# Kernel tuning notes

Hardware: AMD Instinct MI355X
Metric: run time of the kernel (lower is better)

The kernel has to match this reference:

```python
import jax, jax.numpy as jnp
import numpy as np

B, C, T, H, W = 8, 3, 16, 64, 64
CIN = C * T          # 48, conv in_channels
CQK = CIN // 8       # 6, query/key channels


def setup_inputs() -> dict:
    key = jax.random.key(0)
    ks = jax.random.split(key, 8)
    s = 0.05
    return {
        "x": jax.random.normal(ks[0], (B, C, T, H, W), dtype=jnp.float32),
        "Wq": jax.random.normal(ks[1], (CQK, CIN), dtype=jnp.float32) * s,
        "bq": jax.random.normal(ks[2], (CQK,), dtype=jnp.float32) * s,
        "Wk": jax.random.normal(ks[3], (CQK, CIN), dtype=jnp.float32) * s,
        "bk": jax.random.normal(ks[4], (CQK,), dtype=jnp.float32) * s,
        "Wv": jax.random.normal(ks[5], (CIN, CIN), dtype=jnp.float32) * s,
        "bv": jax.random.normal(ks[6], (CIN,), dtype=jnp.float32) * s,
        "gamma": jax.random.normal(ks[7], (1,), dtype=jnp.float32) * s,
    }


def reference(x, Wq, bq, Wk, bk, Wv, bv, gamma):
    b, c, t, h, w = x.shape
    n = h * w
    # merge channel and time dims: [B, C*T, H*W]
    x2 = x.reshape(b, c * t, n)
    # 1x1 convs are per-position channel matmuls
    q = jnp.einsum('oc,bcn->bon', Wq, x2) + bq[None, :, None]   # [B, CQK, N]
    k = jnp.einsum('oc,bcn->bon', Wk, x2) + bk[None, :, None]   # [B, CQK, N]
    v = jnp.einsum('oc,bcn->bon', Wv, x2) + bv[None, :, None]   # [B, CIN, N]
    # energy[b, i, j] = <q[:, i], k[:, j]>
    energy = jnp.einsum('bci,bcj->bij', q, k)                   # [B, N, N]
    attn = jax.nn.softmax(energy, axis=-1)
    # out[b, c, i] = sum_j v[b, c, j] * attn[b, i, j]
    out = jnp.einsum('bcj,bij->bci', v, attn)                   # [B, CIN, N]
    out = gamma[0] * out + x2
    return out.reshape(b, c, t, h, w)
```

## Files before the change

kernel.cpp:

```cpp
#include <hip/hip_runtime.h>

#define B_    8
#define CIN   48
#define CQK   6
#define N_    4096
#define CV    64
#define TI    64
#define TJ    64
#define NCH   4
#define JCH   (N_ / NCH)
#define TILES (JCH / TJ)
#define LOG2E 1.4426950408889634f

typedef __attribute__((ext_vector_type(8)))  short short8;
typedef __attribute__((ext_vector_type(16))) float f32x16;

__device__ __forceinline__ unsigned short f2bf(float f) {
    unsigned int u = __float_as_uint(f);
    u += 0x7FFFu + ((u >> 16) & 1u);
    return (unsigned short)(u >> 16);
}

__device__ __forceinline__ float exp2_fast(float x) {
    float r;
    asm("v_exp_f32 %0, %1" : "=v"(r) : "v"(x));
    return r;
}

__device__ __forceinline__ unsigned int cvt_pk_bf16(float a, float b) {
    unsigned int r;
    asm("v_cvt_pk_bf16_f32 %0, %1, %2" : "=v"(r) : "v"(a), "v"(b));
    return r;
}

__device__ __forceinline__ void pl32swap(unsigned int& x, unsigned int& y) {
    asm("v_permlane32_swap_b32 %0, %1" : "+v"(x), "+v"(y));
}

__device__ __forceinline__ short8 mk8(unsigned int w0, unsigned int w1,
                                      unsigned int w2, unsigned int w3) {
    union { unsigned int u[4]; short8 s; } t;
    t.u[0] = w0; t.u[1] = w1; t.u[2] = w2; t.u[3] = w3;
    return t.s;
}

__device__ __forceinline__ void cp16(const unsigned short* g, unsigned short* l) {
    __builtin_amdgcn_global_load_lds(
        (const __attribute__((address_space(1))) unsigned int*)g,
        (__attribute__((address_space(3))) unsigned int*)l, 16, 0, 0);
}

__global__ __launch_bounds__(256) void qkv_kernel(
    const float* __restrict__ x,
    const float* __restrict__ Wq, const float* __restrict__ bq,
    const float* __restrict__ Wk, const float* __restrict__ bk,
    const float* __restrict__ Wv, const float* __restrict__ bv,
    unsigned short* __restrict__ qB, unsigned short* __restrict__ kB,
    unsigned short* __restrict__ vB)
{
    __shared__ float sWq[CQK * CIN], sWk[CQK * CIN], sWv[CIN * CIN];
    __shared__ float sbq[CQK], sbk[CQK], sbv[CIN];
    const int tid = threadIdx.x;
    for (int idx = tid; idx < CQK * CIN; idx += 256) { sWq[idx] = Wq[idx]; sWk[idx] = Wk[idx]; }
    for (int idx = tid; idx < CIN * CIN; idx += 256) sWv[idx] = Wv[idx];
    if (tid < CQK) { sbq[tid] = bq[tid]; sbk[tid] = bk[tid]; }
    if (tid < CIN) sbv[tid] = bv[tid];
    __syncthreads();

    const int b = blockIdx.x >> 5;
    const int n = ((blockIdx.x & 31) << 7) + (tid & 127);
    const int h = tid >> 7;

    float xc[CIN];
    const float* xb = x + ((size_t)b * CIN) * N_ + n;
#pragma unroll
    for (int c = 0; c < CIN; ++c) xc[c] = xb[(size_t)c * N_];

    if (h == 0) {
        short8 qrow = {0,0,0,0,0,0,0,0}, krow = {0,0,0,0,0,0,0,0};
#pragma unroll
        for (int o = 0; o < CQK; ++o) {
            float sq = sbq[o], sk = sbk[o];
#pragma unroll
            for (int c = 0; c < CIN; ++c) {
                sq += sWq[o * CIN + c] * xc[c];
                sk += sWk[o * CIN + c] * xc[c];
            }
            qrow[o] = (short)f2bf(sq);
            krow[o] = (short)f2bf(sk * LOG2E);
        }
        *(short8*)&qB[((size_t)b * N_ + n) * 8] = qrow;
        *(short8*)&kB[((size_t)b * N_ + n) * 8] = krow;
        vB[((size_t)b * CV + 48) * N_ + n] = 0x3F80u;
#pragma unroll
        for (int o = 49; o < CV; ++o) vB[((size_t)b * CV + o) * N_ + n] = 0;
#pragma unroll
        for (int o = 0; o < 20; ++o) {
            float sv = sbv[o];
#pragma unroll
            for (int c = 0; c < CIN; ++c) sv += sWv[o * CIN + c] * xc[c];
            vB[((size_t)b * CV + o) * N_ + n] = f2bf(sv);
        }
    } else {
#pragma unroll
        for (int o = 20; o < CIN; ++o) {
            float sv = sbv[o];
#pragma unroll
            for (int c = 0; c < CIN; ++c) sv += sWv[o * CIN + c] * xc[c];
            vB[((size_t)b * CV + o) * N_ + n] = f2bf(sv);
        }
    }
}

__global__ __launch_bounds__(512, 4) void attn_kernel(
    const unsigned short* __restrict__ qB, const unsigned short* __restrict__ kB,
    const unsigned short* __restrict__ vB, const float* __restrict__ x,
    const float* __restrict__ gamma, float* __restrict__ out)
{
    __shared__ __align__(16) unsigned short vt[2][NCH][CV][TJ];
    float (*cbuf)[TI + 1] = (float (*)[TI + 1]) & vt[0][0][0][0];

    const int tid   = threadIdx.x;
    const int l     = tid & 63;
    const int w     = tid >> 6;
    const int chunk = w & 3;
    const int iw    = w >> 2;
    const int hi    = l >> 5;
    const int li    = l & 31;
    const int b     = blockIdx.x & 7;
    const int ig    = blockIdx.x >> 3;
    const int i_base = ig * TI;
    const int gx    = (l & 7) ^ ((l >> 3) & 7);

    const unsigned short* kg = kB + (size_t)b * N_ * 8;
    const unsigned short* vg = vB + (size_t)b * CV * N_;

    short8 qf = {0,0,0,0,0,0,0,0};
    if (hi == 0)
        qf = *(const short8*)&qB[((size_t)b * N_ + i_base + iw * 32 + li) * 8];

    f32x16 zc, acc0, acc1;
#pragma unroll
    for (int r = 0; r < 16; ++r) { zc[r] = 0.f; acc0[r] = 0.f; acc1[r] = 0.f; }

#define STAGE(BF, J0)                                                          \
    {                                                                          \
        _Pragma("unroll")                                                      \
        for (int s = 0; s < 4; ++s) {                                          \
            const int c = iw * 32 + s * 8 + (l >> 3);                          \
            cp16(&vg[(size_t)c * N_ + (J0) + gx * 8],                          \
                 &vt[BF][chunk][iw * 32 + s * 8][0]);                          \
        }                                                                      \
    }

#define DO_JST(JST, KF, VTC)                                                   \
    {                                                                          \
        f32x16 s = __builtin_amdgcn_mfma_f32_32x32x16_bf16(KF, qf, zc, 0, 0, 0);\
        _Pragma("unroll")                                                      \
        for (int r = 0; r < 16; ++r) s[r] = exp2_fast(s[r]);                   \
        unsigned int c00 = cvt_pk_bf16(s[0],  s[1]);                           \
        unsigned int c10 = cvt_pk_bf16(s[2],  s[3]);                           \
        unsigned int c01 = cvt_pk_bf16(s[4],  s[5]);                           \
        unsigned int c11 = cvt_pk_bf16(s[6],  s[7]);                           \
        unsigned int c02 = cvt_pk_bf16(s[8],  s[9]);                           \
        unsigned int c12 = cvt_pk_bf16(s[10], s[11]);                          \
        unsigned int c03 = cvt_pk_bf16(s[12], s[13]);                          \
        unsigned int c13 = cvt_pk_bf16(s[14], s[15]);                          \
        unsigned int x0 = c00, y0 = c01; pl32swap(x0, y0);                     \
        unsigned int x1 = c10, y1 = c11; pl32swap(x1, y1);                     \
        const short8 pa0 = mk8(x0, x1, y0, y1);                                \
        unsigned int x2 = c02, y2 = c03; pl32swap(x2, y2);                     \
        unsigned int x3 = c12, y3 = c13; pl32swap(x3, y3);                     \
        const short8 pa1 = mk8(x2, x3, y2, y3);                                \
        const char* vrow0 = (const char*)&(VTC)[li][0];                        \
        const char* vrow1 = (const char*)&(VTC)[32 + li][0];                   \
        short8 vf;                                                             \
        vf = *(const short8*)(vrow0 + ((((JST)*4 + 0 + hi) ^ (li & 7)) << 4)); \
        acc0 = __builtin_amdgcn_mfma_f32_32x32x16_bf16(pa0, vf, acc0, 0, 0, 0);\
        vf = *(const short8*)(vrow0 + ((((JST)*4 + 2 + hi) ^ (li & 7)) << 4)); \
        acc0 = __builtin_amdgcn_mfma_f32_32x32x16_bf16(pa1, vf, acc0, 0, 0, 0);\
        vf = *(const short8*)(vrow1 + ((((JST)*4 + 0 + hi) ^ (li & 7)) << 4)); \
        acc1 = __builtin_amdgcn_mfma_f32_32x32x16_bf16(pa0, vf, acc1, 0, 0, 0);\
        vf = *(const short8*)(vrow1 + ((((JST)*4 + 2 + hi) ^ (li & 7)) << 4)); \
        acc1 = __builtin_amdgcn_mfma_f32_32x32x16_bf16(pa1, vf, acc1, 0, 0, 0);\
    }

    const int jbase = chunk * JCH;
    short8 kf0  = {0,0,0,0,0,0,0,0}, kf1  = {0,0,0,0,0,0,0,0};
    short8 kf0n = {0,0,0,0,0,0,0,0}, kf1n = {0,0,0,0,0,0,0,0};
    STAGE(0, jbase)
    if (hi == 0) {
        kf0 = *(const short8*)&kg[(size_t)(jbase + li) * 8];
        kf1 = *(const short8*)&kg[(size_t)(jbase + 32 + li) * 8];
    }

#pragma unroll 1
    for (int t = 0; t < TILES; ++t) {
        const int bf = t & 1;
        asm volatile("s_waitcnt vmcnt(0)" ::: "memory");
        __builtin_amdgcn_s_barrier();
        __builtin_amdgcn_sched_barrier(0);
        if (t + 1 < TILES) {
            const int j0n = jbase + (t + 1) * TJ;
            STAGE(bf ^ 1, j0n)
            if (hi == 0) {
                kf0n = *(const short8*)&kg[(size_t)(j0n + li) * 8];
                kf1n = *(const short8*)&kg[(size_t)(j0n + 32 + li) * 8];
            }
        }
        __builtin_amdgcn_s_setprio(1);
        DO_JST(0, kf0, vt[bf][chunk])
        DO_JST(1, kf1, vt[bf][chunk])
        __builtin_amdgcn_s_setprio(0);
        kf0 = kf0n; kf1 = kf1n;
    }
#undef DO_JST
#undef STAGE

    __syncthreads();

#pragma unroll 1
    for (int r = 0; r < NCH; ++r) {
        if (chunk == r) {
#pragma unroll
            for (int reg = 0; reg < 16; ++reg) {
                const int i_loc = iw * 32 + (reg & 3) + 8 * (reg >> 2) + 4 * hi;
                if (r == 0) {
                    cbuf[li][i_loc]      = acc0[reg];
                    cbuf[32 + li][i_loc] = acc1[reg];
                } else {
                    cbuf[li][i_loc]      += acc0[reg];
                    cbuf[32 + li][i_loc] += acc1[reg];
                }
            }
        }
        __syncthreads();
    }

    const float gm = gamma[0];
#pragma unroll
    for (int rep = 0; rep < 8; ++rep) {
        const int idx = tid + rep * 512;
        const int c   = idx >> 6;
        const int i2  = idx & 63;
        if (c < CIN) {
            const size_t off = ((size_t)b * CIN + c) * N_ + i_base + i2;
            out[off] = gm * (cbuf[c][i2] / cbuf[48][i2]) + x[off];
        }
    }
}

extern "C" void kernel_launch(void* const* d_in, const int* in_sizes, int n_in,
                              void* d_out, int out_size, void* d_ws, size_t ws_size,
                              hipStream_t stream)
{
    const float* x     = (const float*)d_in[0];
    const float* Wq    = (const float*)d_in[1];
    const float* bq    = (const float*)d_in[2];
    const float* Wk    = (const float*)d_in[3];
    const float* bk    = (const float*)d_in[4];
    const float* Wv    = (const float*)d_in[5];
    const float* bv    = (const float*)d_in[6];
    const float* gamma = (const float*)d_in[7];
    float* out = (float*)d_out;

    unsigned short* qB = (unsigned short*)d_ws;
    unsigned short* kB = qB + (size_t)B_ * N_ * 8;
    unsigned short* vB = kB + (size_t)B_ * N_ * 8;

    qkv_kernel<<<dim3(B_ * 32), dim3(256), 0, stream>>>(
        x, Wq, bq, Wk, bk, Wv, bv, qB, kB, vB);
    attn_kernel<<<dim3(B_ * 64), dim3(512), 0, stream>>>(
        qB, kB, vB, x, gamma, out);
}
```

Before: 51.01 us.

## Stage x tile in LDS and split QKV projection across four wave groups

The QKV projection kernel now loads a 48x64 slice of x into shared memory with float4 loads instead of keeping 48 values per thread in registers. It launches twice as many blocks, each covering 64 positions, and gives one wave the Q/K/padding work and three waves 16 V channels each, which balances the 20/28 split used before. In the attention loop the hand-written waitcnt, barrier and sched_barrier sequence is replaced by __syncthreads, which may change how the compiler schedules around the barrier. mk8 now uses bit_cast, which is cosmetic.

```diff
diff --git a/kernel.cpp b/kernel.cpp
--- a/kernel.cpp
+++ b/kernel.cpp
@@ -13,6 +13,7 @@
 #define LOG2E 1.4426950408889634f
 
 typedef __attribute__((ext_vector_type(8)))  short short8;
+typedef __attribute__((ext_vector_type(4)))  unsigned int uint4v;
 typedef __attribute__((ext_vector_type(16))) float f32x16;
 
 __device__ __forceinline__ unsigned short f2bf(float f) {
@@ -39,9 +40,8 @@
 
 __device__ __forceinline__ short8 mk8(unsigned int w0, unsigned int w1,
                                       unsigned int w2, unsigned int w3) {
-    union { unsigned int u[4]; short8 s; } t;
-    t.u[0] = w0; t.u[1] = w1; t.u[2] = w2; t.u[3] = w3;
-    return t.s;
+    uint4v t = {w0, w1, w2, w3};
+    return __builtin_bit_cast(short8, t);
 }
 
 __device__ __forceinline__ void cp16(const unsigned short* g, unsigned short* l) {
@@ -60,31 +60,39 @@
 {
     __shared__ float sWq[CQK * CIN], sWk[CQK * CIN], sWv[CIN * CIN];
     __shared__ float sbq[CQK], sbk[CQK], sbv[CIN];
+    __shared__ float sx[CIN][64];
     const int tid = threadIdx.x;
     for (int idx = tid; idx < CQK * CIN; idx += 256) { sWq[idx] = Wq[idx]; sWk[idx] = Wk[idx]; }
     for (int idx = tid; idx < CIN * CIN; idx += 256) sWv[idx] = Wv[idx];
     if (tid < CQK) { sbq[tid] = bq[tid]; sbk[tid] = bk[tid]; }
     if (tid < CIN) sbv[tid] = bv[tid];
+
+    const int b  = blockIdx.x >> 6;
+    const int n0 = (blockIdx.x & 63) << 6;
+
+#pragma unroll
+    for (int idx = tid; idx < CIN * 16; idx += 256) {
+        const int c  = idx >> 4;
+        const int j4 = (idx & 15) << 2;
+        *(float4*)&sx[c][j4] =
+            *(const float4*)&x[((size_t)b * CIN + c) * N_ + n0 + j4];
+    }
     __syncthreads();
 
-    const int b = blockIdx.x >> 5;
-    const int n = ((blockIdx.x & 31) << 7) + (tid & 127);
-    const int h = tid >> 7;
-
-    float xc[CIN];
-    const float* xb = x + ((size_t)b * CIN) * N_ + n;
-#pragma unroll
-    for (int c = 0; c < CIN; ++c) xc[c] = xb[(size_t)c * N_];
-
-    if (h == 0) {
+    const int g  = tid >> 6;
+    const int jl = tid & 63;
+    const int n  = n0 + jl;
+
+    if (g == 0) {
         short8 qrow = {0,0,0,0,0,0,0,0}, krow = {0,0,0,0,0,0,0,0};
 #pragma unroll
         for (int o = 0; o < CQK; ++o) {
             float sq = sbq[o], sk = sbk[o];
 #pragma unroll
             for (int c = 0; c < CIN; ++c) {
-                sq += sWq[o * CIN + c] * xc[c];
-                sk += sWk[o * CIN + c] * xc[c];
+                const float xv = sx[c][jl];
+                sq += sWq[o * CIN + c] * xv;
+                sk += sWk[o * CIN + c] * xv;
             }
             qrow[o] = (short)f2bf(sq);
             krow[o] = (short)f2bf(sk * LOG2E);
@@ -94,19 +102,14 @@
         vB[((size_t)b * CV + 48) * N_ + n] = 0x3F80u;
 #pragma unroll
         for (int o = 49; o < CV; ++o) vB[((size_t)b * CV + o) * N_ + n] = 0;
-#pragma unroll
-        for (int o = 0; o < 20; ++o) {
+    } else {
+        const int o0 = (g - 1) * 16;
+#pragma unroll
+        for (int oo = 0; oo < 16; ++oo) {
+            const int o = o0 + oo;
             float sv = sbv[o];
 #pragma unroll
-            for (int c = 0; c < CIN; ++c) sv += sWv[o * CIN + c] * xc[c];
-            vB[((size_t)b * CV + o) * N_ + n] = f2bf(sv);
-        }
-    } else {
-#pragma unroll
-        for (int o = 20; o < CIN; ++o) {
-            float sv = sbv[o];
-#pragma unroll
-            for (int c = 0; c < CIN; ++c) sv += sWv[o * CIN + c] * xc[c];
+            for (int c = 0; c < CIN; ++c) sv += sWv[o * CIN + c] * sx[c][jl];
             vB[((size_t)b * CV + o) * N_ + n] = f2bf(sv);
         }
     }
@@ -197,9 +200,7 @@
 #pragma unroll 1
     for (int t = 0; t < TILES; ++t) {
         const int bf = t & 1;
-        asm volatile("s_waitcnt vmcnt(0)" ::: "memory");
-        __builtin_amdgcn_s_barrier();
-        __builtin_amdgcn_sched_barrier(0);
+        __syncthreads();
         if (t + 1 < TILES) {
             const int j0n = jbase + (t + 1) * TJ;
             STAGE(bf ^ 1, j0n)
@@ -268,7 +269,7 @@
     unsigned short* kB = qB + (size_t)B_ * N_ * 8;
     unsigned short* vB = kB + (size_t)B_ * N_ * 8;
 
-    qkv_kernel<<<dim3(B_ * 32), dim3(256), 0, stream>>>(
+    qkv_kernel<<<dim3(B_ * 64), dim3(256), 0, stream>>>(
         x, Wq, bq, Wk, bk, Wv, bv, qB, kB, vB);
     attn_kernel<<<dim3(B_ * 64), dim3(512), 0, stream>>>(
         qB, kB, vB, x, gamma, out);
```

After: 50.42 us (median of 2 runs). No clear change (-1.2%).
